# Kernel tuning notes

Measured on AMD Instinct MI355X. Metric: run time of the kernel, lower is better.

## Reference

```python
import jax, jax.numpy as jnp
import numpy as np


def setup_inputs() -> dict:
    key = jax.random.key(0)
    k1, k2, k3 = jax.random.split(key, 3)
    B, Ci, Co, H, W, M1, M2 = 16, 64, 64, 256, 256, 16, 16
    scale = 1.0 / (Ci * Co)
    x = jax.random.normal(k1, (B, Ci, H, W), dtype=jnp.float32)
    # weights stored as real view of complex [Ci, Co, M1, M2] -> trailing dim 2
    weights1 = scale * jax.random.uniform(k2, (Ci, Co, M1, M2, 2), dtype=jnp.float32)
    weights2 = scale * jax.random.uniform(k3, (Ci, Co, M1, M2, 2), dtype=jnp.float32)
    return {"x": x, "weights1": weights1, "weights2": weights2}


def reference(x, weights1, weights2):
    B, Ci, H, W = x.shape
    Co, M1, M2 = weights1.shape[1], weights1.shape[2], weights1.shape[3]
    Wf = W // 2 + 1

    # FFT over spatial dims -> [B, Ci, H, W//2+1] complex64
    x_ft = jnp.fft.rfft2(x)

    w1 = jax.lax.complex(weights1[..., 0], weights1[..., 1])
    w2 = jax.lax.complex(weights2[..., 0], weights2[..., 1])

    # truncated complex mode mixing over channels
    top = jnp.einsum('bixy,ioxy->boxy', x_ft[:, :, :M1, :M2], w1)
    bot = jnp.einsum('bixy,ioxy->boxy', x_ft[:, :, H - M1:, :M2], w2)

    out_ft = jnp.zeros((B, Co, H, Wf), dtype=x_ft.dtype)
    out_ft = out_ft.at[:, :, :M1, :M2].set(top)
    out_ft = out_ft.at[:, :, H - M1:, :M2].set(bot)

    return jnp.fft.irfft2(out_ft, s=(H, W))
```

## Files before the change

### kernel.cpp

```cpp
#include <hip/hip_runtime.h>
#include <math.h>

#define PI2f 6.28318530717958647692f


static constexpr size_t REG = 65536;
static constexpr size_t TW_ABS = 32768;

__global__ __launch_bounds__(256) void prep2(const float* __restrict__ w1,
                                             const float* __restrict__ w2,
                                             float* __restrict__ g) {
    const int b = blockIdx.x;
    const int t = threadIdx.x;
    if (b < 512) {
        __shared__ float ws[16 * 516];
        const int wsel = b >> 8;
        const int iob = b & 255;
        const float* src = (wsel ? w2 : w1) + (size_t)iob * 16 * 512;
#pragma unroll
        for (int q = 0; q < 8; q++) {
            int fid = q * 256 + t;
            int row = fid >> 7, c = fid & 127;
            float4 v = *(const float4*)(src + (size_t)row * 512 + c * 4);
            *(float4*)(ws + row * 516 + c * 4) = v;
        }
        __syncthreads();
        const int m = t + (wsel << 8);
        float* dst = g + (size_t)m * REG + 4096 + (size_t)iob * 32;
#pragma unroll
        for (int rq = 0; rq < 8; rq++) {
            int r = rq * 2;
            float2 a  = *(const float2*)(ws + r * 516 + 2 * t);
            float2 bv = *(const float2*)(ws + (r + 1) * 516 + 2 * t);
            *(float4*)(dst + rq * 4) = make_float4(a.x, a.y, bv.x, bv.y);
        }
    } else {
        int idx = (b - 512) * 256 + t;
        int w = idx >> 4, k = idx & 15;
        int r = (w * k) & 255;
        float s, c;
        sincosf(PI2f * (float)r / 256.0f, &s, &c);
        g[TW_ABS + (size_t)idx * 2]     = c;
        g[TW_ABS + (size_t)idx * 2 + 1] = -s;
    }
}

__global__ __launch_bounds__(256, 4) void fwd(const float* __restrict__ x,
                                              const float* __restrict__ twg,
                                              float* __restrict__ g) {
    __shared__ float As[16 * 516 + 4];
    const int t = threadIdx.x;
    const int bi = blockIdx.x;
    const float* xrow = x + (size_t)bi * 65536 + (size_t)t * 256;

    float ar[16], ai[16];
#pragma unroll
    for (int k = 0; k < 16; k++) { ar[k] = 0.f; ai[k] = 0.f; }

    for (int a = 0; a < 4; a++) {
        float4 lo[8], hi[8];
#pragma unroll
        for (int q = 0; q < 8; q++) lo[q] = *(const float4*)(xrow + a * 32 + q * 4);
#pragma unroll
        for (int q = 0; q < 8; q++) hi[q] = *(const float4*)(xrow + a * 32 + 128 + q * 4);
#pragma unroll
        for (int q = 0; q < 8; q++) {
            float xe[4], xo[4];
            xe[0] = lo[q].x + hi[q].x; xo[0] = lo[q].x - hi[q].x;
            xe[1] = lo[q].y + hi[q].y; xo[1] = lo[q].y - hi[q].y;
            xe[2] = lo[q].z + hi[q].z; xo[2] = lo[q].z - hi[q].z;
            xe[3] = lo[q].w + hi[q].w; xo[3] = lo[q].w - hi[q].w;
#pragma unroll
            for (int e = 0; e < 4; e++) {
                const int w = a * 32 + q * 4 + e;
                const float* tp = twg + w * 32;
#pragma unroll
                for (int k = 0; k < 16; k++) {
                    float xv = (k & 1) ? xo[e] : xe[e];
                    ar[k] = fmaf(xv, tp[2 * k],     ar[k]);
                    ai[k] = fmaf(xv, tp[2 * k + 1], ai[k]);
                }
            }
        }
    }
#pragma unroll
    for (int k = 0; k < 16; k++) {
        *(float2*)(As + k * 516 + t * 2) = make_float2(ar[k], ai[k]);
    }
    __syncthreads();

    const int k = t & 15, jb = t >> 4;
    const float* Ak = As + k * 516;
    float* Xp = g + (size_t)bi * REG + 2048;
    for (int half = 0; half < 2; half++) {
        int j = jb + half * 16;
        int f = (j < 16) ? j : j - 32;
        float s, c;
        sincosf(-PI2f * (float)f / 256.0f, &s, &c);
        float er = 1.f, ei = 0.f, accr = 0.f, acci = 0.f;
        for (int h = 0; h < 256; h += 2) {
            float4 a2 = *(const float4*)(Ak + 2 * h);
            accr = fmaf(a2.x, er, fmaf(-a2.y, ei, accr));
            acci = fmaf(a2.x, ei, fmaf( a2.y, er, acci));
            float nr = er * c - ei * s;
            ei = fmaf(er, s, ei * c);
            er = nr;
            accr = fmaf(a2.z, er, fmaf(-a2.w, ei, accr));
            acci = fmaf(a2.z, ei, fmaf( a2.w, er, acci));
            nr = er * c - ei * s;
            ei = fmaf(er, s, ei * c);
            er = nr;
        }
        *(float2*)(Xp + ((size_t)j * 16 + k) * 2) = make_float2(accr, acci);
    }
}

__global__ __launch_bounds__(256, 4) void mix2(float* __restrict__ g) {
    __shared__ float Ws[8192];
    __shared__ float Xs[2048];
    const int m = blockIdx.x;
    const int t = threadIdx.x;
    const float* Wp = g + (size_t)m * REG + 4096;
#pragma unroll
    for (int q = 0; q < 8; q++) {
        int fid = q * 256 + t;
        *(float4*)(Ws + fid * 4) = *(const float4*)(Wp + (size_t)fid * 4);
    }
#pragma unroll
    for (int q = 0; q < 4; q++) {
        int bi = q * 256 + t;
        float2 v = *(const float2*)(g + (size_t)bi * REG + 2048 + (size_t)m * 2);
        *(float2*)(Xs + bi * 2) = v;
    }
    __syncthreads();

    const int b = t >> 4, og = t & 15;
    float acr[4] = {0.f, 0.f, 0.f, 0.f}, aci[4] = {0.f, 0.f, 0.f, 0.f};
    const float* Wb = Ws + og * 8;
    const float* Xb = Xs + b * 128;
    for (int i = 0; i < 64; i++) {
        float2 xv = *(const float2*)(Xb + 2 * i);
        float4 w0 = *(const float4*)(Wb + i * 128);
        float4 w1v = *(const float4*)(Wb + i * 128 + 4);
        acr[0] = fmaf(xv.x, w0.x, fmaf(-xv.y, w0.y, acr[0]));
        aci[0] = fmaf(xv.x, w0.y, fmaf( xv.y, w0.x, aci[0]));
        acr[1] = fmaf(xv.x, w0.z, fmaf(-xv.y, w0.w, acr[1]));
        aci[1] = fmaf(xv.x, w0.w, fmaf( xv.y, w0.z, aci[1]));
        acr[2] = fmaf(xv.x, w1v.x, fmaf(-xv.y, w1v.y, acr[2]));
        aci[2] = fmaf(xv.x, w1v.y, fmaf( xv.y, w1v.x, aci[2]));
        acr[3] = fmaf(xv.x, w1v.z, fmaf(-xv.y, w1v.w, acr[3]));
        aci[3] = fmaf(xv.x, w1v.w, fmaf( xv.y, w1v.z, aci[3]));
    }
#pragma unroll
    for (int oo = 0; oo < 4; oo++) {
        int o = og * 4 + oo;
        *(float2*)(g + (size_t)(b * 64 + o) * REG + (size_t)m * 2) = make_float2(acr[oo], aci[oo]);
    }
}

__global__ __launch_bounds__(256, 4) void inv_fused(float* __restrict__ g) {
    __shared__ float Fs[1024];
    __shared__ float phS[512];
    __shared__ float T[256 * 32];
    const int t = threadIdx.x;
    const int bo = blockIdx.x;
    float* regn = g + (size_t)bo * REG;

    *(float4*)(Fs + t * 4) = *(const float4*)(regn + (size_t)t * 4);
    float rs, rc;
    sincosf(PI2f * (float)t / 256.0f, &rs, &rc);
    phS[t * 2] = rc; phS[t * 2 + 1] = rs;
    __syncthreads();

    float Yr[16], Yi[16];
#pragma unroll
    for (int k = 0; k < 16; k++) { Yr[k] = 0.f; Yi[k] = 0.f; }
    float es, ec;
    sincosf(-PI2f * (float)(t & 15) / 16.0f, &es, &ec);
    float er = ec, ei = es;
    for (int sdx = 0; sdx < 32; sdx++) {
        int j = (sdx < 16) ? sdx + 16 : sdx - 16;
        const float* fj = Fs + j * 32;
#pragma unroll
        for (int kq = 0; kq < 8; kq++) {
            float4 fv = *(const float4*)(fj + 4 * kq);
            Yr[2 * kq]     = fmaf(fv.x, er, fmaf(-fv.y, ei, Yr[2 * kq]));
            Yi[2 * kq]     = fmaf(fv.x, ei, fmaf( fv.y, er, Yi[2 * kq]));
            Yr[2 * kq + 1] = fmaf(fv.z, er, fmaf(-fv.w, ei, Yr[2 * kq + 1]));
            Yi[2 * kq + 1] = fmaf(fv.z, ei, fmaf( fv.w, er, Yi[2 * kq + 1]));
        }
        float nr = er * rc - ei * rs;
        ei = fmaf(er, rs, ei * rc);
        er = nr;
    }

    const float INV = 1.0f / 65536.0f;
    Yr[0] *= INV;
#pragma unroll
    for (int k = 1; k < 16; k++) { Yr[k] *= 2.0f * INV; Yi[k] *= 2.0f * INV; }

    auto pq = [&](float c, float s, float& P, float& Q) {
        float c2 = c + c;
        float Cp = c, Cpp = 1.f, Sp = s, Spp = 0.f;
        P = fmaf(Yr[1], c, Yr[0]);
        Q = Yi[1] * s;
#pragma unroll
        for (int k = 2; k < 16; k++) {
            float Cn = fmaf(c2, Cp, -Cpp);
            float Sn = fmaf(c2, Sp, -Spp);
            P = fmaf(Yr[k], Cn, P);
            Q = fmaf(Yi[k], Sn, Q);
            Cpp = Cp; Cp = Cn; Spp = Sp; Sp = Sn;
        }
    };

    const int sw = t & 7;
    const int rsub = t >> 3, f4 = t & 7;
    for (int a = 0; a < 8; a++) {
        float val[32];
#pragma unroll
        for (int q = 0; q < 32; q++) {
            int col = a * 32 + q;
            int m = (a < 4) ? col : 256 - col;
            float P, Q;
            pq(phS[2 * m], phS[2 * m + 1], P, Q);
            val[q] = (a < 4) ? (P - Q) : (P + Q);
        }
        __syncthreads();
        float* Tr = T + t * 32;
#pragma unroll
        for (int q4 = 0; q4 < 8; q4++) {
            *(float4*)(Tr + ((q4 ^ sw) * 4)) =
                make_float4(val[q4 * 4], val[q4 * 4 + 1], val[q4 * 4 + 2], val[q4 * 4 + 3]);
        }
        __syncthreads();
#pragma unroll
        for (int it = 0; it < 8; it++) {
            int row = it * 32 + rsub;
            float4 v = *(const float4*)(T + row * 32 + ((f4 ^ (row & 7)) * 4));
            *(float4*)(regn + (size_t)row * 256 + a * 32 + f4 * 4) = v;
        }
    }
}

extern "C" void kernel_launch(void* const* d_in, const int* in_sizes, int n_in,
                              void* d_out, int out_size, void* d_ws, size_t ws_size,
                              hipStream_t stream) {
    const float* x  = (const float*)d_in[0];
    const float* w1 = (const float*)d_in[1];
    const float* w2 = (const float*)d_in[2];
    float* g = (float*)d_out;
    (void)d_ws; (void)ws_size;

    prep2    <<<528,  256, 0, stream>>>(w1, w2, g);
    fwd      <<<1024, 256, 0, stream>>>(x, g + TW_ABS, g);
    mix2     <<<512,  256, 0, stream>>>(g);
    inv_fused<<<1024, 256, 0, stream>>>(g);
}
```

Baseline: 238.7 us.

## Apply radix-4 folding to forward row DFT and fold column DFT halves

The forward kernel's row DFT now folds the input with a radix-4 butterfly (E, F, D, G) before accumulating the 16 low modes, using twiddle symmetries so the multiply count is roughly halved. The column DFT pass now combines rows h and h+128 with a sign that depends on mode parity, and computes both frequency halves in a single loop over 128 rows rather than two separate 256-row loops. This cuts FMA work and shared-memory reads in the fwd kernel. It adds more live registers and relies on the sign trick, which assumes (f1 - f2) equals 16, and on exact twiddle symmetry.

```diff
diff --git a/kernel.cpp b/kernel.cpp
--- a/kernel.cpp
+++ b/kernel.cpp
@@ -57,29 +57,38 @@
 #pragma unroll
     for (int k = 0; k < 16; k++) { ar[k] = 0.f; ai[k] = 0.f; }
 
-    for (int a = 0; a < 4; a++) {
-        float4 lo[8], hi[8];
-#pragma unroll
-        for (int q = 0; q < 8; q++) lo[q] = *(const float4*)(xrow + a * 32 + q * 4);
-#pragma unroll
-        for (int q = 0; q < 8; q++) hi[q] = *(const float4*)(xrow + a * 32 + 128 + q * 4);
-#pragma unroll
-        for (int q = 0; q < 8; q++) {
-            float xe[4], xo[4];
-            xe[0] = lo[q].x + hi[q].x; xo[0] = lo[q].x - hi[q].x;
-            xe[1] = lo[q].y + hi[q].y; xo[1] = lo[q].y - hi[q].y;
-            xe[2] = lo[q].z + hi[q].z; xo[2] = lo[q].z - hi[q].z;
-            xe[3] = lo[q].w + hi[q].w; xo[3] = lo[q].w - hi[q].w;
-#pragma unroll
-            for (int e = 0; e < 4; e++) {
-                const int w = a * 32 + q * 4 + e;
-                const float* tp = twg + w * 32;
-#pragma unroll
-                for (int k = 0; k < 16; k++) {
-                    float xv = (k & 1) ? xo[e] : xe[e];
-                    ar[k] = fmaf(xv, tp[2 * k],     ar[k]);
-                    ai[k] = fmaf(xv, tp[2 * k + 1], ai[k]);
-                }
+#pragma unroll 4
+    for (int q = 0; q < 16; q++) {
+        float4 x0 = *(const float4*)(xrow + q * 4);
+        float4 x1 = *(const float4*)(xrow + q * 4 + 64);
+        float4 x2 = *(const float4*)(xrow + q * 4 + 128);
+        float4 x3 = *(const float4*)(xrow + q * 4 + 192);
+        float E[4], F[4], D[4], G[4];
+        E[0] = x0.x + x2.x; F[0] = x1.x + x3.x; D[0] = x0.x - x2.x; G[0] = x1.x - x3.x;
+        E[1] = x0.y + x2.y; F[1] = x1.y + x3.y; D[1] = x0.y - x2.y; G[1] = x1.y - x3.y;
+        E[2] = x0.z + x2.z; F[2] = x1.z + x3.z; D[2] = x0.z - x2.z; G[2] = x1.z - x3.z;
+        E[3] = x0.w + x2.w; F[3] = x1.w + x3.w; D[3] = x0.w - x2.w; G[3] = x1.w - x3.w;
+#pragma unroll
+        for (int e = 0; e < 4; e++) {
+            const int w1 = q * 4 + e;
+            const float* tp = twg + w1 * 32;
+            float sEF = E[e] + F[e], dEF = E[e] - F[e];
+#pragma unroll
+            for (int kk = 0; kk < 4; kk++) {
+                int k0 = 4 * kk;
+                ar[k0] = fmaf(sEF, tp[2 * k0],     ar[k0]);
+                ai[k0] = fmaf(sEF, tp[2 * k0 + 1], ai[k0]);
+                int k2 = 4 * kk + 2;
+                ar[k2] = fmaf(dEF, tp[2 * k2],     ar[k2]);
+                ai[k2] = fmaf(dEF, tp[2 * k2 + 1], ai[k2]);
+                int k1 = 4 * kk + 1;
+                float c1 = tp[2 * k1], s1 = tp[2 * k1 + 1];
+                ar[k1] = fmaf(D[e], c1, fmaf( G[e], s1, ar[k1]));
+                ai[k1] = fmaf(D[e], s1, fmaf(-G[e], c1, ai[k1]));
+                int k3 = 4 * kk + 3;
+                float c3 = tp[2 * k3], s3 = tp[2 * k3 + 1];
+                ar[k3] = fmaf(D[e], c3, fmaf(-G[e], s3, ar[k3]));
+                ai[k3] = fmaf(D[e], s3, fmaf( G[e], c3, ai[k3]));
             }
         }
     }
@@ -92,27 +101,35 @@
     const int k = t & 15, jb = t >> 4;
     const float* Ak = As + k * 516;
     float* Xp = g + (size_t)bi * REG + 2048;
-    for (int half = 0; half < 2; half++) {
-        int j = jb + half * 16;
-        int f = (j < 16) ? j : j - 32;
-        float s, c;
-        sincosf(-PI2f * (float)f / 256.0f, &s, &c);
-        float er = 1.f, ei = 0.f, accr = 0.f, acci = 0.f;
-        for (int h = 0; h < 256; h += 2) {
-            float4 a2 = *(const float4*)(Ak + 2 * h);
-            accr = fmaf(a2.x, er, fmaf(-a2.y, ei, accr));
-            acci = fmaf(a2.x, ei, fmaf( a2.y, er, acci));
-            float nr = er * c - ei * s;
-            ei = fmaf(er, s, ei * c);
-            er = nr;
-            accr = fmaf(a2.z, er, fmaf(-a2.w, ei, accr));
-            acci = fmaf(a2.z, ei, fmaf( a2.w, er, acci));
-            nr = er * c - ei * s;
-            ei = fmaf(er, s, ei * c);
-            er = nr;
-        }
-        *(float2*)(Xp + ((size_t)j * 16 + k) * 2) = make_float2(accr, acci);
-    }
+    const int f1 = jb;
+    const int f2 = jb - 16;
+    const float sgn = (jb & 1) ? -1.0f : 1.0f;
+    float s1, c1, s2, c2;
+    sincosf(-PI2f * (float)f1 / 256.0f, &s1, &c1);
+    sincosf(-PI2f * (float)f2 / 256.0f, &s2, &c2);
+    float e1r = 1.f, e1i = 0.f, a1r = 0.f, a1i = 0.f;
+    float e2r = 1.f, e2i = 0.f, a2r = 0.f, a2i = 0.f;
+    for (int hp = 0; hp < 128; hp += 2) {
+        float4 lo = *(const float4*)(Ak + 2 * hp);
+        float4 hi = *(const float4*)(Ak + 2 * (hp + 128));
+#pragma unroll
+        for (int e = 0; e < 2; e++) {
+            float cr = (e ? lo.z : lo.x) + sgn * (e ? hi.z : hi.x);
+            float ci = (e ? lo.w : lo.y) + sgn * (e ? hi.w : hi.y);
+            a1r = fmaf(cr, e1r, fmaf(-ci, e1i, a1r));
+            a1i = fmaf(cr, e1i, fmaf( ci, e1r, a1i));
+            float n1 = e1r * c1 - e1i * s1;
+            e1i = fmaf(e1r, s1, e1i * c1);
+            e1r = n1;
+            a2r = fmaf(cr, e2r, fmaf(-ci, e2i, a2r));
+            a2i = fmaf(cr, e2i, fmaf( ci, e2r, a2i));
+            float n2 = e2r * c2 - e2i * s2;
+            e2i = fmaf(e2r, s2, e2i * c2);
+            e2r = n2;
+        }
+    }
+    *(float2*)(Xp + ((size_t)jb * 16 + k) * 2)        = make_float2(a1r, a1i);
+    *(float2*)(Xp + ((size_t)(jb + 16) * 16 + k) * 2) = make_float2(a2r, a2i);
 }
 
 __global__ __launch_bounds__(256, 4) void mix2(float* __restrict__ g) {
```

Result: slower. 248.4 us (+4.1%).
